# Kernel optimization log

Measured on AMD Instinct MI355X. Metric: run time of the kernel, lower is better.

Reference implementation:

```python
import jax, jax.numpy as jnp
import numpy as np

B, T, H, D = 4, 2048, 16, 64
HID = H * D
ROPE_THETA = 10000.0


def _rope_tables(t, d, theta):
    # frequencies over half the head dim, duplicated to full head_dim
    inv_freq = 1.0 / (theta ** (np.arange(0, d, 2, dtype=np.float32) / d))  # (d/2,)
    pos = np.arange(t, dtype=np.float32)
    freqs = np.outer(pos, inv_freq)                      # (T, d/2)
    emb = np.concatenate([freqs, freqs], axis=-1)        # (T, d)
    return jnp.asarray(np.cos(emb)), jnp.asarray(np.sin(emb))


def setup_inputs() -> dict:
    key = jax.random.key(0)
    ks = jax.random.split(key, 5)
    s = 1.0 / np.sqrt(HID)
    cos, sin = _rope_tables(T, D, ROPE_THETA)
    return {
        "x": jax.random.normal(ks[0], (B, T, HID), dtype=jnp.float32),
        "cos": cos,
        "sin": sin,
        "wq": jax.random.normal(ks[1], (HID, HID), dtype=jnp.float32) * s,
        "wk": jax.random.normal(ks[2], (HID, HID), dtype=jnp.float32) * s,
        "wv": jax.random.normal(ks[3], (HID, HID), dtype=jnp.float32) * s,
        "wo": jax.random.normal(ks[4], (HID, HID), dtype=jnp.float32) * s,
    }


def _rotate_half(x):
    x1, x2 = jnp.split(x, 2, axis=-1)
    return jnp.concatenate([-x2, x1], axis=-1)


def reference(x, cos, sin, wq, wk, wv, wo):
    b, t, _ = x.shape
    # QKV projections (nn.Linear: y = x @ W^T), reshape to (B, H, T, D)
    q = (x @ wq.T).reshape(b, t, H, D).transpose(0, 2, 1, 3)
    k = (x @ wk.T).reshape(b, t, H, D).transpose(0, 2, 1, 3)
    v = (x @ wv.T).reshape(b, t, H, D).transpose(0, 2, 1, 3)
    # RoPE
    c = cos[None, None, :, :]
    s = sin[None, None, :, :]
    q = q * c + _rotate_half(q) * s
    k = k * c + _rotate_half(k) * s
    # causal SDPA
    scale = 1.0 / jnp.sqrt(jnp.asarray(D, dtype=x.dtype))
    scores = jnp.einsum("bhqd,bhkd->bhqk", q, k) * scale
    causal = jnp.tril(jnp.ones((t, t), dtype=bool))
    scores = jnp.where(causal[None, None], scores, jnp.finfo(scores.dtype).min)
    attn = jax.nn.softmax(scores, axis=-1)
    out = jnp.einsum("bhqk,bhkd->bhqd", attn, v)
    out = out.transpose(0, 2, 1, 3).reshape(b, t, HID)
    return out @ wo.T
```

## Files before the change

### kernel.cpp

```cpp
#include <hip/hip_runtime.h>

#define BSZ 4
#define TT 2048
#define NH 16
#define HD 64
#define HID 1024
#define BT 8192
#define BH 64

typedef unsigned short u16;
typedef unsigned int u32;
typedef unsigned long long u64;
typedef __attribute__((ext_vector_type(4))) float f32x4;
typedef __attribute__((ext_vector_type(8))) short bf16x8;

#define MFMA32(a, b, c) __builtin_amdgcn_mfma_f32_16x16x32_bf16(a, b, c, 0, 0, 0)

typedef const __attribute__((address_space(1))) u32* gp32;
typedef __attribute__((address_space(3))) u32* lp32;

__device__ __forceinline__ u16 f2bf(float f) {
    union { float f; u32 u; } x; x.f = f;
    u32 r = x.u + 0x7FFFu + ((x.u >> 16) & 1u);
    return (u16)(r >> 16);
}

__global__ __launch_bounds__(256) void cast_kernel(const float* __restrict__ src,
                                                   u16* __restrict__ dst, int n4) {
    int i = blockIdx.x * 256 + threadIdx.x;
    if (i >= n4) return;
    f32x4 v = *(const f32x4*)(src + (size_t)i * 4);
    uint2 u;
    u.x = (u32)f2bf(v[0]) | ((u32)f2bf(v[1]) << 16);
    u.y = (u32)f2bf(v[2]) | ((u32)f2bf(v[3]) << 16);
    *(uint2*)(dst + (size_t)i * 4) = u;
}

template<int MODE>
__global__ __launch_bounds__(256)
void gemm_bt(const u16* __restrict__ A, const u16* __restrict__ W,
             float* __restrict__ Cf, u16* __restrict__ qkv, u16* __restrict__ vt,
             const float* __restrict__ cosT, const float* __restrict__ sinT) {
    __shared__ u16 sh[128 * 128];
    u16* As = sh;
    u16* Bs = sh + 128 * 64;
    const int tid  = threadIdx.x;
    const int wv   = tid >> 6, lane = tid & 63;
    const int lrow = lane & 15, lk = lane >> 4;
    const int wm   = (wv & 1) * 64, wn = (wv >> 1) * 64;
    const int m0   = blockIdx.x * 128, n0 = blockIdx.y * 128;

    f32x4 acc[4][4] = {};

    for (int kk = 0; kk < HID; kk += 64) {
        __syncthreads();
        #pragma unroll
        for (int i = 0; i < 4; ++i) {
            int l16 = i * 256 + tid;
            int r = l16 >> 3, c = l16 & 7;
            int gc = (c ^ (r & 7)) * 8;
            __builtin_amdgcn_global_load_lds(
                (gp32)&A[(size_t)(m0 + r) * HID + kk + gc],
                (lp32)&As[l16 * 8], 16, 0, 0);
            __builtin_amdgcn_global_load_lds(
                (gp32)&W[(size_t)(n0 + r) * HID + kk + gc],
                (lp32)&Bs[l16 * 8], 16, 0, 0);
        }
        __syncthreads();

        #pragma unroll
        for (int k0 = 0; k0 < 64; k0 += 32) {
            bf16x8 af[4], bfr[4];
            #pragma unroll
            for (int i = 0; i < 4; ++i) {
                int row = wm + i * 16 + lrow;
                int pc  = ((k0 >> 3) + lk) ^ (row & 7);
                af[i] = *(const bf16x8*)&As[row * 64 + pc * 8];
            }
            #pragma unroll
            for (int j = 0; j < 4; ++j) {
                int row = wn + j * 16 + lrow;
                int pc  = ((k0 >> 3) + lk) ^ (row & 7);
                bfr[j] = *(const bf16x8*)&Bs[row * 64 + pc * 8];
            }
            #pragma unroll
            for (int i = 0; i < 4; ++i)
                #pragma unroll
                for (int j = 0; j < 4; ++j)
                    acc[i][j] = MFMA32(af[i], bfr[j], acc[i][j]);
        }
    }
    __syncthreads();

    if (MODE == 0) {
        if (blockIdx.y < 16) {
            const float QSC = (blockIdx.y < 8) ? 0.125f * 1.44269504f : 1.0f;
            #pragma unroll
            for (int i = 0; i < 4; ++i)
                #pragma unroll
                for (int r = 0; r < 4; ++r) {
                    int tl = (m0 + wm + i * 16 + lk * 4 + r) & (TT - 1);
                    #pragma unroll
                    for (int j = 0; j < 2; ++j) {
                        int dd = j * 16 + lrow;
                        float c = cosT[tl * HD + dd], s = sinT[tl * HD + dd];
                        float v1 = acc[i][j][r], v2 = acc[i][j + 2][r];
                        acc[i][j][r]     = (v1 * c - v2 * s) * QSC;
                        acc[i][j + 2][r] = (v2 * c + v1 * s) * QSC;
                    }
                }
        }
        #pragma unroll
        for (int i = 0; i < 4; ++i)
            #pragma unroll
            for (int j = 0; j < 4; ++j)
                #pragma unroll
                for (int r = 0; r < 4; ++r)
                    sh[(wm + i * 16 + lk * 4 + r) * 128 + wn + j * 16 + lrow] = f2bf(acc[i][j][r]);
        __syncthreads();
        const int b = m0 >> 11, tl0 = m0 & (TT - 1);
        if (blockIdx.y < 16) {
            #pragma unroll
            for (int p = 0; p < 8; ++p) {
                int idx = p * 256 + tid;
                int r = idx >> 4, c16 = idx & 15;
                f32x4 v = *(const f32x4*)&sh[r * 128 + c16 * 8];
                int nfull = n0 + c16 * 8;
                int proj = nfull >> 10, nl = nfull & 1023;
                int h = nl >> 6, d = nl & 63;
                u16* dst = qkv + (size_t)proj * BT * HID +
                           (((size_t)(b * NH + h) * TT + tl0 + r) * HD + d);
                *(f32x4*)dst = v;
            }
        } else {
            #pragma unroll
            for (int p = 0; p < 8; ++p) {
                int oc  = p * 256 + tid;
                int col = oc & 127;
                int t8  = oc >> 7;
                union { f32x4 v4; u16 u[8]; } u;
                #pragma unroll
                for (int j = 0; j < 8; ++j) u.u[j] = sh[(t8 * 8 + j) * 128 + col];
                int nl = ((n0 - 2048) + col);
                int h = nl >> 6, d = nl & 63;
                *(f32x4*)&vt[((size_t)(b * NH + h) * HD + d) * TT + tl0 + t8 * 8] = u.v4;
            }
        }
    } else {
        #pragma unroll
        for (int i = 0; i < 4; ++i)
            #pragma unroll
            for (int j = 0; j < 4; ++j)
                #pragma unroll
                for (int r = 0; r < 4; ++r) {
                    int m = m0 + wm + i * 16 + lk * 4 + r;
                    int n = n0 + wn + j * 16 + lrow;
                    Cf[(size_t)m * HID + n] = acc[i][j][r];
                }
    }
}

__device__ __forceinline__ u32 cvtpk(float lo, float hi) {
    u32 r;
    asm("v_cvt_pk_bf16_f32 %0, %1, %2" : "=v"(r) : "v"(lo), "v"(hi));
    return r;
}
__device__ __forceinline__ bf16x8 packP(const f32x4& a, const f32x4& b) {
    union { bf16x8 v; u32 w[4]; } u;
    u.w[0] = cvtpk(a[0], a[1]); u.w[1] = cvtpk(a[2], a[3]);
    u.w[2] = cvtpk(b[0], b[1]); u.w[3] = cvtpk(b[2], b[3]);
    return u.v;
}

#define VST 68

__global__ __launch_bounds__(256)
void attn_kernel(const u16* __restrict__ q, const u16* __restrict__ k,
                 const u16* __restrict__ vt, u16* __restrict__ o) {
    __shared__ u16 Ks[64 * 72];
    __shared__ u16 Vts[64 * VST];
    const int tid  = threadIdx.x;
    const int w    = tid >> 6, lane = tid & 63;
    const int lrow = lane & 15, lk = lane >> 4;
    const int nlid = (blockIdx.x & 7) * 128 + (blockIdx.x >> 3);
    const int p    = nlid & 15;
    const int bh   = nlid >> 4;
    const int q0a  = 64 * p, q0b = 64 * (31 - p);
    const size_t hb = (size_t)bh * TT * HD;

    bf16x8 qfa[2], qfb[2];
    #pragma unroll
    for (int kq = 0; kq < 2; ++kq) {
        qfa[kq] = *(const bf16x8*)&q[hb + (size_t)(q0a + w * 16 + lrow) * HD + kq * 32 + lk * 8];
        qfb[kq] = *(const bf16x8*)&q[hb + (size_t)(q0b + w * 16 + lrow) * HD + kq * 32 + lk * 8];
    }

    f32x4 oa[4] = {}, obc[4] = {};
    float lia = 0.f, lib = 0.f;

    const int r0 = tid >> 3, f0 = (tid & 7) * 8;
    const int r1 = (tid + 256) >> 3, f1 = (tid & 7) * 8;

    f32x4 pk0 = *(const f32x4*)&k[hb + (size_t)r0 * HD + f0];
    f32x4 pk1 = *(const f32x4*)&k[hb + (size_t)r1 * HD + f1];
    f32x4 pv0 = *(const f32x4*)&vt[hb + (size_t)r0 * TT + f0];
    f32x4 pv1 = *(const f32x4*)&vt[hb + (size_t)r1 * TT + f1];

    const int nIter = 32 - p;
    for (int it = 0; it < nIter; ++it) {
        const bool a_act = (it <= p);
        __syncthreads();
        *(f32x4*)&Ks[r0 * 72 + f0]   = pk0;
        *(f32x4*)&Ks[r1 * 72 + f1]   = pk1;
        *(f32x4*)&Vts[r0 * VST + f0] = pv0;
        *(f32x4*)&Vts[r1 * VST + f1] = pv1;
        __syncthreads();
        if (it + 1 < nIter) {
            const int nn = (it + 1) * 64;
            pk0 = *(const f32x4*)&k[hb + (size_t)(nn + r0) * HD + f0];
            pk1 = *(const f32x4*)&k[hb + (size_t)(nn + r1) * HD + f1];
            pv0 = *(const f32x4*)&vt[hb + (size_t)r0 * TT + nn + f0];
            pv1 = *(const f32x4*)&vt[hb + (size_t)r1 * TT + nn + f1];
        }

        bf16x8 kf0[4], kf1[4];
        #pragma unroll
        for (int mt = 0; mt < 4; ++mt) {
            kf0[mt] = *(const bf16x8*)&Ks[(mt * 16 + lrow) * 72 + lk * 8];
            kf1[mt] = *(const bf16x8*)&Ks[(mt * 16 + lrow) * 72 + 32 + lk * 8];
        }

        {
            f32x4 s[4] = {};
            __builtin_amdgcn_s_setprio(1);
            #pragma unroll
            for (int mt = 0; mt < 4; ++mt) {
                s[mt] = MFMA32(kf0[mt], qfb[0], s[mt]);
                s[mt] = MFMA32(kf1[mt], qfb[1], s[mt]);
            }
            __builtin_amdgcn_s_setprio(0);
            if (it == nIter - 1) {
                #pragma unroll
                for (int mt = 0; mt < 4; ++mt)
                    #pragma unroll
                    for (int r = 0; r < 4; ++r)
                        if (mt * 16 + lk * 4 + r > w * 16 + lrow) s[mt][r] = -1e30f;
            }
            #pragma unroll
            for (int mt = 0; mt < 4; ++mt)
                #pragma unroll
                for (int r = 0; r < 4; ++r) {
                    float pv = exp2f(s[mt][r]);
                    s[mt][r] = pv; lib += pv;
                }
            bf16x8 p0 = packP(s[0], s[1]), p1 = packP(s[2], s[3]);
            __builtin_amdgcn_s_setprio(1);
            #pragma unroll
            for (int t2 = 0; t2 < 2; ++t2)
                #pragma unroll
                for (int dm = 0; dm < 4; ++dm) {
                    union { bf16x8 v; struct { u64 lo, hi; } u; } vf;
                    const u16* vrow = &Vts[(dm * 16 + lrow) * VST + t2 * 32 + lk * 4];
                    vf.u.lo = *(const u64*)vrow;
                    vf.u.hi = *(const u64*)(vrow + 16);
                    obc[dm] = MFMA32(vf.v, t2 ? p1 : p0, obc[dm]);
                }
            __builtin_amdgcn_s_setprio(0);
        }

        if (a_act) {
            f32x4 s[4] = {};
            __builtin_amdgcn_s_setprio(1);
            #pragma unroll
            for (int mt = 0; mt < 4; ++mt) {
                s[mt] = MFMA32(kf0[mt], qfa[0], s[mt]);
                s[mt] = MFMA32(kf1[mt], qfa[1], s[mt]);
            }
            __builtin_amdgcn_s_setprio(0);
            if (it == p) {
                #pragma unroll
                for (int mt = 0; mt < 4; ++mt)
                    #pragma unroll
                    for (int r = 0; r < 4; ++r)
                        if (mt * 16 + lk * 4 + r > w * 16 + lrow) s[mt][r] = -1e30f;
            }
            #pragma unroll
            for (int mt = 0; mt < 4; ++mt)
                #pragma unroll
                for (int r = 0; r < 4; ++r) {
                    float pv = exp2f(s[mt][r]);
                    s[mt][r] = pv; lia += pv;
                }
            bf16x8 p0 = packP(s[0], s[1]), p1 = packP(s[2], s[3]);
            __builtin_amdgcn_s_setprio(1);
            #pragma unroll
            for (int t2 = 0; t2 < 2; ++t2)
                #pragma unroll
                for (int dm = 0; dm < 4; ++dm) {
                    union { bf16x8 v; struct { u64 lo, hi; } u; } vf;
                    const u16* vrow = &Vts[(dm * 16 + lrow) * VST + t2 * 32 + lk * 4];
                    vf.u.lo = *(const u64*)vrow;
                    vf.u.hi = *(const u64*)(vrow + 16);
                    oa[dm] = MFMA32(vf.v, t2 ? p1 : p0, oa[dm]);
                }
            __builtin_amdgcn_s_setprio(0);
        }
    }

    lia += __shfl_xor(lia, 16, 64); lia += __shfl_xor(lia, 32, 64);
    lib += __shfl_xor(lib, 16, 64); lib += __shfl_xor(lib, 32, 64);
    const int b = bh >> 4, h = bh & 15;
    const float inva = 1.f / lia, invb = 1.f / lib;
    #pragma unroll
    for (int dm = 0; dm < 4; ++dm) {
        uint2 pk;
        pk.x = cvtpk(oa[dm][0] * inva, oa[dm][1] * inva);
        pk.y = cvtpk(oa[dm][2] * inva, oa[dm][3] * inva);
        int row = q0a + w * 16 + lrow;
        *(uint2*)&o[((size_t)(b * TT + row)) * HID + h * HD + dm * 16 + lk * 4] = pk;
        pk.x = cvtpk(obc[dm][0] * invb, obc[dm][1] * invb);
        pk.y = cvtpk(obc[dm][2] * invb, obc[dm][3] * invb);
        row = q0b + w * 16 + lrow;
        *(uint2*)&o[((size_t)(b * TT + row)) * HID + h * HD + dm * 16 + lk * 4] = pk;
    }
}

extern "C" void kernel_launch(void* const* d_in, const int* in_sizes, int n_in,
                              void* d_out, int out_size, void* d_ws, size_t ws_size,
                              hipStream_t stream) {
    const float* x    = (const float*)d_in[0];
    const float* cosT = (const float*)d_in[1];
    const float* sinT = (const float*)d_in[2];
    const float* wq   = (const float*)d_in[3];
    const float* wk   = (const float*)d_in[4];
    const float* wv   = (const float*)d_in[5];
    const float* wo   = (const float*)d_in[6];
    float* out = (float*)d_out;

    char* ws = (char*)d_ws;
    size_t off = 0;
    u16* x_bf  = (u16*)(ws + off); off += (size_t)BT * HID * 2;
    u16* wqkv  = (u16*)(ws + off); off += (size_t)3 * HID * HID * 2;
    u16* wo_bf = (u16*)(ws + off); off += (size_t)HID * HID * 2;
    u16* qb    = (u16*)(ws + off); off += (size_t)BT * HID * 2;
    u16* kb    = (u16*)(ws + off); off += (size_t)BT * HID * 2;
    u16* vtb   = (u16*)(ws + off); off += (size_t)BT * HID * 2;
    u16* ob    = (u16*)(ws + off); off += (size_t)BT * HID * 2;
    (void)kb;

    cast_kernel<<<(BT * HID / 4 + 255) / 256, 256, 0, stream>>>(x, x_bf, BT * HID / 4);
    cast_kernel<<<1024, 256, 0, stream>>>(wq, wqkv, HID * HID / 4);
    cast_kernel<<<1024, 256, 0, stream>>>(wk, wqkv + (size_t)HID * HID, HID * HID / 4);
    cast_kernel<<<1024, 256, 0, stream>>>(wv, wqkv + (size_t)2 * HID * HID, HID * HID / 4);
    cast_kernel<<<1024, 256, 0, stream>>>(wo, wo_bf, HID * HID / 4);

    gemm_bt<0><<<dim3(BT / 128, 3 * HID / 128), 256, 0, stream>>>(
        x_bf, wqkv, nullptr, qb, vtb, cosT, sinT);

    attn_kernel<<<dim3(1024), 256, 0, stream>>>(qb, kb, vtb, ob);

    gemm_bt<1><<<dim3(BT / 128, HID / 128), 256, 0, stream>>>(
        ob, wo_bf, out, nullptr, nullptr, nullptr, nullptr);
}
```

Measured before the change: 279.4 us.

## Triple-buffer GEMM loads with 256x128 tiles, 8 waves, and padded epilogue

Reworks the bf16 GEMM into 512-thread blocks that each compute a 256x128 tile. Global-to-LDS loads for the tile two K-steps ahead are issued into a 3-stage ring buffer, interleaved with MFMA work, and controlled by explicit vmcnt waits, barriers and setprio. This is meant to hide load latency that the old single-buffer, sync-then-compute loop exposed. The epilogue now uses padded LDS strides, and the V-transpose path stores V already transposed so it can do vector reads. The cost is more LDS (about 144KB per block) and hand-tuned wait counts that must stay in step with the number of loads issued.

```diff
diff --git a/kernel.cpp b/kernel.cpp
--- a/kernel.cpp
+++ b/kernel.cpp
@@ -37,62 +37,96 @@
 }
 
 template<int MODE>
-__global__ __launch_bounds__(256)
+__global__ __launch_bounds__(512, 2)
 void gemm_bt(const u16* __restrict__ A, const u16* __restrict__ W,
              float* __restrict__ Cf, u16* __restrict__ qkv, u16* __restrict__ vt,
              const float* __restrict__ cosT, const float* __restrict__ sinT) {
-    __shared__ u16 sh[128 * 128];
-    u16* As = sh;
-    u16* Bs = sh + 128 * 64;
+    __shared__ __align__(16) u16 sh[3 * 24576];
     const int tid  = threadIdx.x;
-    const int wv   = tid >> 6, lane = tid & 63;
+    const int wid  = tid >> 6, lane = tid & 63;
     const int lrow = lane & 15, lk = lane >> 4;
-    const int wm   = (wv & 1) * 64, wn = (wv >> 1) * 64;
-    const int m0   = blockIdx.x * 128, n0 = blockIdx.y * 128;
-
-    f32x4 acc[4][4] = {};
-
-    for (int kk = 0; kk < HID; kk += 64) {
-        __syncthreads();
+    const int wm   = (wid >> 1) * 64, wn = (wid & 1) * 64;
+    const int m0   = blockIdx.x * 256, n0 = blockIdx.y * 128;
+
+    auto stageA = [&](int buf, int kk, int half) {
+        u16* dst = sh + buf * 24576;
         #pragma unroll
-        for (int i = 0; i < 4; ++i) {
-            int l16 = i * 256 + tid;
+        for (int s = 0; s < 2; ++s) {
+            int l16 = half * 1024 + s * 512 + tid;
             int r = l16 >> 3, c = l16 & 7;
             int gc = (c ^ (r & 7)) * 8;
             __builtin_amdgcn_global_load_lds(
                 (gp32)&A[(size_t)(m0 + r) * HID + kk + gc],
-                (lp32)&As[l16 * 8], 16, 0, 0);
+                (lp32)&dst[l16 * 8], 16, 0, 0);
+        }
+    };
+    auto stageB = [&](int buf, int kk) {
+        u16* dst = sh + buf * 24576 + 16384;
+        #pragma unroll
+        for (int s = 0; s < 2; ++s) {
+            int l16 = s * 512 + tid;
+            int r = l16 >> 3, c = l16 & 7;
+            int gc = (c ^ (r & 7)) * 8;
             __builtin_amdgcn_global_load_lds(
                 (gp32)&W[(size_t)(n0 + r) * HID + kk + gc],
-                (lp32)&Bs[l16 * 8], 16, 0, 0);
-        }
-        __syncthreads();
+                (lp32)&dst[l16 * 8], 16, 0, 0);
+        }
+    };
+
+    f32x4 acc[4][4] = {};
+
+    stageA(0, 0, 0); stageA(0, 0, 1); stageB(0, 0);
+    stageA(1, 64, 0); stageA(1, 64, 1); stageB(1, 64);
+
+    int b = 0;
+    for (int t = 0; t < 16; ++t) {
+        if (t < 15) asm volatile("s_waitcnt vmcnt(6)" ::: "memory");
+        else        asm volatile("s_waitcnt vmcnt(0)" ::: "memory");
+        __builtin_amdgcn_s_barrier();
+        const u16* As = sh + b * 24576;
+        const u16* Bs = As + 16384;
+        int b2 = b + 2; if (b2 >= 3) b2 -= 3;
+        const bool st  = (t + 2 < 16);
+        const int kk2  = (t + 2) * 64;
 
         #pragma unroll
-        for (int k0 = 0; k0 < 64; k0 += 32) {
+        for (int h = 0; h < 2; ++h) {
             bf16x8 af[4], bfr[4];
             #pragma unroll
             for (int i = 0; i < 4; ++i) {
                 int row = wm + i * 16 + lrow;
-                int pc  = ((k0 >> 3) + lk) ^ (row & 7);
+                int pc  = (h * 4 + lk) ^ (row & 7);
                 af[i] = *(const bf16x8*)&As[row * 64 + pc * 8];
             }
             #pragma unroll
             for (int j = 0; j < 4; ++j) {
                 int row = wn + j * 16 + lrow;
-                int pc  = ((k0 >> 3) + lk) ^ (row & 7);
+                int pc  = (h * 4 + lk) ^ (row & 7);
                 bfr[j] = *(const bf16x8*)&Bs[row * 64 + pc * 8];
             }
+            if (st) {
+                if (h == 0) { stageA(b2, kk2, 0); stageB(b2, kk2); }
+                else        { stageA(b2, kk2, 1); }
+            }
+            __builtin_amdgcn_s_barrier();
+            asm volatile("s_waitcnt lgkmcnt(0)" ::: "memory");
+            __builtin_amdgcn_sched_barrier(0);
+            __builtin_amdgcn_s_setprio(1);
             #pragma unroll
             for (int i = 0; i < 4; ++i)
                 #pragma unroll
                 for (int j = 0; j < 4; ++j)
                     acc[i][j] = MFMA32(af[i], bfr[j], acc[i][j]);
-        }
+            __builtin_amdgcn_s_setprio(0);
+            __builtin_amdgcn_sched_barrier(0);
+            __builtin_amdgcn_s_barrier();
+        }
+        ++b; if (b == 3) b = 0;
     }
     __syncthreads();
 
     if (MODE == 0) {
+        const int bb = m0 >> 11, tl0 = m0 & (TT - 1);
         if (blockIdx.y < 16) {
             const float QSC = (blockIdx.y < 8) ? 0.125f * 1.44269504f : 1.0f;
             #pragma unroll
@@ -109,41 +143,46 @@
                         acc[i][j + 2][r] = (v2 * c + v1 * s) * QSC;
                     }
                 }
-        }
-        #pragma unroll
-        for (int i = 0; i < 4; ++i)
-            #pragma unroll
-            for (int j = 0; j < 4; ++j)
-                #pragma unroll
-                for (int r = 0; r < 4; ++r)
-                    sh[(wm + i * 16 + lk * 4 + r) * 128 + wn + j * 16 + lrow] = f2bf(acc[i][j][r]);
-        __syncthreads();
-        const int b = m0 >> 11, tl0 = m0 & (TT - 1);
-        if (blockIdx.y < 16) {
+            #pragma unroll
+            for (int i = 0; i < 4; ++i)
+                #pragma unroll
+                for (int j = 0; j < 4; ++j)
+                    #pragma unroll
+                    for (int r = 0; r < 4; ++r)
+                        sh[(wm + i * 16 + lk * 4 + r) * 136 + wn + j * 16 + lrow] =
+                            f2bf(acc[i][j][r]);
+            __syncthreads();
             #pragma unroll
             for (int p = 0; p < 8; ++p) {
-                int idx = p * 256 + tid;
+                int idx = p * 512 + tid;
                 int r = idx >> 4, c16 = idx & 15;
-                f32x4 v = *(const f32x4*)&sh[r * 128 + c16 * 8];
+                f32x4 v = *(const f32x4*)&sh[r * 136 + c16 * 8];
                 int nfull = n0 + c16 * 8;
                 int proj = nfull >> 10, nl = nfull & 1023;
                 int h = nl >> 6, d = nl & 63;
                 u16* dst = qkv + (size_t)proj * BT * HID +
-                           (((size_t)(b * NH + h) * TT + tl0 + r) * HD + d);
+                           (((size_t)(bb * NH + h) * TT + tl0 + r) * HD + d);
                 *(f32x4*)dst = v;
             }
         } else {
             #pragma unroll
+            for (int i = 0; i < 4; ++i)
+                #pragma unroll
+                for (int j = 0; j < 4; ++j)
+                    #pragma unroll
+                    for (int r = 0; r < 4; ++r)
+                        sh[(wn + j * 16 + lrow) * 272 + wm + i * 16 + lk * 4 + r] =
+                            f2bf(acc[i][j][r]);
+            __syncthreads();
+            #pragma unroll
             for (int p = 0; p < 8; ++p) {
-                int oc  = p * 256 + tid;
-                int col = oc & 127;
-                int t8  = oc >> 7;
-                union { f32x4 v4; u16 u[8]; } u;
-                #pragma unroll
-                for (int j = 0; j < 8; ++j) u.u[j] = sh[(t8 * 8 + j) * 128 + col];
-                int nl = ((n0 - 2048) + col);
+                int oc  = p * 512 + tid;
+                int t8  = oc & 31;
+                int col = oc >> 5;
+                f32x4 v = *(const f32x4*)&sh[col * 272 + t8 * 8];
+                int nl = (n0 - 2048) + col;
                 int h = nl >> 6, d = nl & 63;
-                *(f32x4*)&vt[((size_t)(b * NH + h) * HD + d) * TT + tl0 + t8 * 8] = u.v4;
+                *(f32x4*)&vt[((size_t)(bb * NH + h) * HD + d) * TT + tl0 + t8 * 8] = v;
             }
         }
     } else {
@@ -354,11 +393,11 @@
     cast_kernel<<<1024, 256, 0, stream>>>(wv, wqkv + (size_t)2 * HID * HID, HID * HID / 4);
     cast_kernel<<<1024, 256, 0, stream>>>(wo, wo_bf, HID * HID / 4);
 
-    gemm_bt<0><<<dim3(BT / 128, 3 * HID / 128), 256, 0, stream>>>(
+    gemm_bt<0><<<dim3(BT / 256, 3 * HID / 128), 512, 0, stream>>>(
         x_bf, wqkv, nullptr, qb, vtb, cosT, sinT);
 
     attn_kernel<<<dim3(1024), 256, 0, stream>>>(qb, kb, vtb, ob);
 
-    gemm_bt<1><<<dim3(BT / 128, HID / 128), 256, 0, stream>>>(
+    gemm_bt<1><<<dim3(BT / 256, HID / 128), 512, 0, stream>>>(
         ob, wo_bf, out, nullptr, nullptr, nullptr, nullptr);
 }
```

Result: faster. 266.8 us (-4.5%).
